# Performance work log

Hardware: AMD Instinct MI355X
Metric: run time of the kernel (lower is better)

Reference implementation:

```python
import jax, jax.numpy as jnp
import numpy as np

EPS = 1e-6
PC_MIN = jnp.array([-50.0, -50.0, -4.0], jnp.float32)
PC_MAX = jnp.array([50.0, 50.0, 4.0], jnp.float32)
IMG_H, IMG_W = 256, 704
G, P, L, D = 1, 8, 4, 128


def _conv3x3(x, w, b):
    y = jax.lax.conv_general_dilated(x, w, (1, 1), ((1, 1), (1, 1)),
                                     dimension_numbers=('NCHW', 'OIHW', 'NCHW'))
    return y + b[None, :, None, None]


def _inorm(x):
    # InstanceNorm2d(affine=False), eps=1e-5, per-sample per-channel over (H,W)
    m = jnp.mean(x, axis=(2, 3), keepdims=True)
    v = jnp.var(x, axis=(2, 3), keepdims=True)
    return (x - m) * jax.lax.rsqrt(v + 1e-5)


def _bilinear(img, xy):
    # img: [H, W, C]; xy: [M, 2] in [0,1] (align_corners=False, zero padding)
    H, W, _ = img.shape
    px = xy[:, 0] * W - 0.5
    py = xy[:, 1] * H - 0.5
    x0 = jnp.floor(px)
    y0 = jnp.floor(py)
    wx = px - x0
    wy = py - y0
    x0 = x0.astype(jnp.int32)
    y0 = y0.astype(jnp.int32)

    def tap(xi, yi, w):
        ok = (xi >= 0) & (xi < W) & (yi >= 0) & (yi < H)
        v = img[jnp.clip(yi, 0, H - 1), jnp.clip(xi, 0, W - 1)]
        return v * (w * ok)[:, None]

    return (tap(x0, y0, (1 - wx) * (1 - wy)) + tap(x0 + 1, y0, wx * (1 - wy)) +
            tap(x0, y0 + 1, (1 - wx) * wy) + tap(x0 + 1, y0 + 1, wx * wy))


def _sampling_4d(pts, feats, scale_w, l2i):
    # pts: [B,Q,G,P,3]; feats: list of [B*G,N,Hl,Wl,C]; scale_w: [B,Q,G,1,P,L]; l2i: [B,N,4,4]
    B, Q, g, p, _ = pts.shape
    N = l2i.shape[1]
    hom = jnp.concatenate([pts, jnp.ones(pts.shape[:-1] + (1,), pts.dtype)], -1)
    cam = jnp.einsum('bnij,bqgpj->bqngpi', l2i, hom)  # project to each camera
    z = cam[..., 2:3]
    xy = cam[..., :2] / jnp.maximum(z, 1e-5)
    xy = xy / jnp.array([IMG_W, IMG_H], xy.dtype)
    xy = jnp.where(z > 1e-5, xy, -1e4)  # behind camera -> samples zero
    xy = jnp.transpose(xy, (0, 3, 2, 1, 4, 5)).reshape(B * g * N, Q * p, 2)
    out = 0.0
    for l, f in enumerate(feats):
        C = f.shape[-1]
        fi = f.reshape(B * g * N, f.shape[2], f.shape[3], C)
        s = jax.vmap(_bilinear)(fi, xy).reshape(B, g, N, Q, p, C).sum(2)  # sum over cameras
        w = jnp.transpose(scale_w[:, :, :, 0, :, l], (0, 2, 1, 3))  # [B,G,Q,P]
        out = out + s * w[..., None]
    return jnp.transpose(out, (0, 2, 1, 3, 4))  # [B,Q,G,P,C]


def _forward(feat0, feat1, feat2, feat3, lidar2img, bev_query, bev_pos,
             in_w, in_b, off_w, off_b, sw_w, sw_b,
             pe_w1, pe_b1, pe_w2, pe_b2,
             mid_w1, mid_b1, mid_w2, mid_b2, mid_w3, mid_b3,
             out_w, out_b):
    B, _, h, w = bev_query.shape
    # decoder prologue: b n (g c) H W -> (b g) n H W c  (G=1)
    feats = [jnp.transpose(f, (0, 1, 3, 4, 2)) for f in (feat0, feat1, feat2, feat3)]
    q = _inorm(bev_query + _conv3x3(bev_query, in_w, in_b))
    qf = jnp.transpose(q, (0, 2, 3, 1)).reshape(B, h * w, D)
    # sampling offsets (1x1 conv as matmul), mode='grid', scale=1.0
    off = jax.nn.sigmoid(qf @ off_w.T + off_b).reshape(B, h * w, G, P, 3)
    lim_xy = 0.25 * 1.0 + EPS
    lim_z = 4.0 + EPS
    off = jnp.concatenate([off[..., :2] * 2 * lim_xy - lim_xy,
                           off[..., 2:3] * 2 * lim_z - lim_z], -1)
    ref = bev_pos.reshape(B, h * w, 1, 1, 3) * (PC_MAX - PC_MIN) + PC_MIN
    pts = ref + off  # [B,Q,G,P,3] in world coords
    sw = (qf @ sw_w.T + sw_b).reshape(B, h * w, G, P, L)[:, :, :, None]  # b q g 1 p l
    sw = jax.nn.softmax(sw, axis=-1)
    sampled = _sampling_4d(pts, feats, sw, lidar2img)  # [B,Q,G,P,128]
    ref_n = (pts - PC_MIN) / (PC_MAX - PC_MIN)
    pe = jax.nn.relu(ref_n @ pe_w1 + pe_b1) @ pe_w2 + pe_b2  # PositionalEncodingMap MLP
    sampled = sampled + pe
    # b (h w) g p c -> b (p g c) h w
    sf = jnp.transpose(sampled, (0, 3, 2, 4, 1)).reshape(B, P * G * 128, h, w)
    m = jax.nn.gelu(jnp.einsum('oi,bihw->bohw', mid_w1, sf) + mid_b1[None, :, None, None], approximate=False)
    m = jax.nn.gelu(jnp.einsum('oi,bihw->bohw', mid_w2, m) + mid_b2[None, :, None, None], approximate=False)
    m = jnp.einsum('oi,bihw->bohw', mid_w3, m) + mid_b3[None, :, None, None]
    q = _inorm(q + m)
    q = _inorm(q + _conv3x3(q, out_w, out_b))
    height = jnp.transpose(off[..., 2], (0, 2, 3, 1)).reshape(B, G, P, h, w)
    return q, height


def _lidar2img_np():
    mats = []
    K = np.array([[500., 0., IMG_W / 2, 0.],
                  [0., 500., IMG_H / 2, 0.],
                  [0., 0., 1., 0.],
                  [0., 0., 0., 1.]])
    for n in range(6):
        th = 2 * np.pi * n / 6
        fwd = np.array([np.cos(th), np.sin(th), 0.])
        right = np.array([-np.sin(th), np.cos(th), 0.])
        down = np.array([0., 0., -1.])
        R = np.stack([right, down, fwd])
        c = fwd * 0.5 + np.array([0., 0., 1.5])
        T = np.eye(4)
        T[:3, :3] = R
        T[:3, 3] = -R @ c
        mats.append(K @ T)
    return np.stack(mats)[None].astype(np.float32)


def setup_inputs():
    key = jax.random.key(0)
    ks = jax.random.split(key, 16)

    def rn(k, shape, s=0.02):
        return jax.random.normal(k, shape, jnp.float32) * s

    B, N, h, w = 1, 6, 128, 128
    return dict(
        feat0=jax.random.normal(ks[0], (B, N, 128, 32, 88), jnp.float32),
        feat1=jax.random.normal(ks[1], (B, N, 128, 16, 44), jnp.float32),
        feat2=jax.random.normal(ks[2], (B, N, 128, 8, 22), jnp.float32),
        feat3=jax.random.normal(ks[3], (B, N, 128, 4, 11), jnp.float32),
        lidar2img=jnp.asarray(_lidar2img_np()),
        bev_query=jax.random.normal(ks[4], (B, 128, h, w), jnp.float32),
        bev_pos=jax.random.uniform(ks[5], (B, h, w, 3), jnp.float32),
        in_w=rn(ks[6], (128, 128, 3, 3)), in_b=jnp.zeros(128, jnp.float32),
        off_w=rn(ks[7], (G * P * 3, 128)),
        off_b=jax.random.uniform(ks[8], (G * P * 3,), jnp.float32, -4.0, 4.0),
        sw_w=rn(ks[9], (G * P * L, 128)), sw_b=jnp.zeros(G * P * L, jnp.float32),
        pe_w1=rn(ks[10], (3, 256), 0.5), pe_b1=jnp.zeros(256, jnp.float32),
        pe_w2=rn(ks[11], (256, 128), 0.1), pe_b2=jnp.zeros(128, jnp.float32),
        mid_w1=rn(ks[12], (512, P * 128)), mid_b1=jnp.zeros(512, jnp.float32),
        mid_w2=rn(ks[13], (512, 512)), mid_b2=jnp.zeros(512, jnp.float32),
        mid_w3=rn(ks[14], (128, 512)), mid_b3=jnp.zeros(128, jnp.float32),
        out_w=rn(ks[15], (128, 128, 3, 3)), out_b=jnp.zeros(128, jnp.float32),
    )


def reference(feat0, feat1, feat2, feat3, lidar2img, bev_query, bev_pos,
              in_w, in_b, off_w, off_b, sw_w, sw_b,
              pe_w1, pe_b1, pe_w2, pe_b2,
              mid_w1, mid_b1, mid_w2, mid_b2, mid_w3, mid_b3,
              out_w, out_b):
    return _forward(feat0, feat1, feat2, feat3, lidar2img, bev_query, bev_pos,
                    in_w, in_b, off_w, off_b, sw_w, sw_b,
                    pe_w1, pe_b1, pe_w2, pe_b2,
                    mid_w1, mid_b1, mid_w2, mid_b2, mid_w3, mid_b3,
                    out_w, out_b)
```

## Files before the change

### kernel.cpp

```cpp
#include <hip/hip_runtime.h>
#include <hip/hip_bf16.h>
#include <math.h>

#define HW 16384

typedef __attribute__((ext_vector_type(8))) short short8;
typedef __attribute__((ext_vector_type(4))) float floatx4;
typedef __attribute__((ext_vector_type(2))) float floatx2;

__device__ __forceinline__ float gelu_exact(float x){
    return 0.5f * x * (1.0f + erff(x * 0.7071067811865475f));
}

__device__ __forceinline__ floatx2 bf2x(unsigned int u){
    floatx2 r;
    r.x = __uint_as_float(u << 16);
    r.y = __uint_as_float(u & 0xffff0000u);
    return r;
}

__global__ __launch_bounds__(256) void feat_transpose_all_k(
    const float* __restrict__ f0, const float* __restrict__ f1,
    const float* __restrict__ f2, const float* __restrict__ f3,
    __hip_bfloat16* __restrict__ out)
{
    int idx = blockIdx.x * 256 + threadIdx.x;
    const float* in; int Hl, Wl, base;
    if (idx < 2162688)      { in = f0; Hl = 32; Wl = 88; base = 0; }
    else if (idx < 2703360) { in = f1; Hl = 16; Wl = 44; base = 2162688; }
    else if (idx < 2838528) { in = f2; Hl = 8;  Wl = 22; base = 2703360; }
    else                    { in = f3; Hl = 4;  Wl = 11; base = 2838528; }
    int r   = idx - base;
    int c   = r & 127;
    int pix = r >> 7;
    int x   = pix % Wl;
    int tt  = pix / Wl;
    int y   = tt % Hl;
    int n   = tt / Hl;
    out[idx] = __float2bfloat16(in[((n * 128 + c) * Hl + y) * Wl + x]);
}

__global__ __launch_bounds__(256) void prep_k(
    const float* __restrict__ mid_w1, const float* __restrict__ mid_w2,
    const float* __restrict__ mid_w3, const float* __restrict__ pe_w2,
    const float* __restrict__ off_w,  const float* __restrict__ off_b,
    const float* __restrict__ sw_w,   const float* __restrict__ sw_b,
    const float* __restrict__ in_w,   const float* __restrict__ out_w,
    __hip_bfloat16* __restrict__ Wb1, __hip_bfloat16* __restrict__ Wb2,
    __hip_bfloat16* __restrict__ Wb3, __hip_bfloat16* __restrict__ Wpe,
    __hip_bfloat16* __restrict__ Wof, float* __restrict__ Bof,
    __hip_bfloat16* __restrict__ Wcv1, __hip_bfloat16* __restrict__ Wcv2)
{
    int b = blockIdx.x, t = threadIdx.x;
    if (b < 2048) {
        int i = b * 256 + t; Wb1[i] = __float2bfloat16(mid_w1[i]);
    } else if (b < 3072) {
        int i = (b - 2048) * 256 + t; Wb2[i] = __float2bfloat16(mid_w2[i]);
    } else if (b < 3328) {
        int i = (b - 3072) * 256 + t; Wb3[i] = __float2bfloat16(mid_w3[i]);
    } else if (b < 3456) {
        int n = b - 3328; Wpe[n * 256 + t] = __float2bfloat16(pe_w2[t * 128 + n]);
    } else if (b < 3584) {
        int n = b - 3456;
        if (t < 128) {
            float w = 0.f;
            if (n < 24)      w = off_w[n * 128 + t];
            else if (n < 56) w = sw_w[(n - 24) * 128 + t];
            Wof[n * 128 + t] = __float2bfloat16(w);
            if (t == 0) Bof[n] = (n < 24) ? off_b[n] : ((n < 56) ? sw_b[n - 24] : 0.f);
        }
    } else if (b < 3712) {
        int o = b - 3584;
        for (int idx = t; idx < 1152; idx += 256) {
            int s = idx >> 7, i = idx & 127;
            Wcv1[o * 1152 + idx] = __float2bfloat16(in_w[(o * 128 + i) * 9 + s]);
        }
    } else {
        int o = b - 3712;
        for (int idx = t; idx < 1152; idx += 256) {
            int s = idx >> 7, i = idx & 127;
            Wcv2[o * 1152 + idx] = __float2bfloat16(out_w[(o * 128 + i) * 9 + s]);
        }
    }
}

__global__ __launch_bounds__(256) void chw2hwc_pad_k(
    const float* __restrict__ q, const float* __restrict__ stats,
    __hip_bfloat16* __restrict__ out)
{
    __shared__ float tile[128][65];
    __shared__ float sm[128], sr[128];
    int t = threadIdx.x;
    if (t < 128) {
        if (stats) {
            float s = stats[2 * t], s2 = stats[2 * t + 1];
            float mean = s * (1.0f / HW);
            sm[t] = mean;
            sr[t] = rsqrtf(s2 * (1.0f / HW) - mean * mean + 1e-5f);
        } else {
            sm[t] = 0.f; sr[t] = 1.f;
        }
    }
    int b = blockIdx.x;
    int y = b >> 1, x0 = (b & 1) * 64;
    int xi = t & 63, c0 = t >> 6;
    for (int c = c0; c < 128; c += 4)
        tile[c][xi] = q[c * HW + y * 128 + x0 + xi];
    __syncthreads();
    int xp = t >> 2, cg = (t & 3) * 32;
    __hip_bfloat16* dst = out + ((size_t)(y + 1) * 130 + (x0 + 1 + xp)) * 128;
    #pragma unroll
    for (int g = 0; g < 4; g++) {
        int c = cg + g * 8;
        union { __hip_bfloat16 h[8]; uint4 u; } pk;
        #pragma unroll
        for (int j = 0; j < 8; j++)
            pk.h[j] = __float2bfloat16((tile[c + j][xp] - sm[c + j]) * sr[c + j]);
        *(uint4*)&dst[c] = pk.u;
    }
}

template<int BM, int BN, int ACT, int OUTT, int CONV>
__global__ __launch_bounds__(256) void bgemm_k(
    const __hip_bfloat16* __restrict__ X, const __hip_bfloat16* __restrict__ W,
    const float* __restrict__ bias, void* __restrict__ outp,
    const float* __restrict__ res,
    const float* __restrict__ rstats, float* __restrict__ ostats,
    int M, int K, int N)
{
    constexpr int ROWS = BM + BN;
    constexpr int ITERS = (ROWS * 4) / 256;
    constexpr int BUFE  = ROWS * 32;
    constexpr int NBUF  = (ITERS == 2) ? 4 : 3;
    __shared__ __align__(16) __hip_bfloat16 SH[NBUF * BUFE];
    int t = threadIdx.x;
    int w = t >> 6, lane = t & 63;
    int mb = blockIdx.y * BM, nb = blockIdx.x * BN;
    int cy = mb >> 7, cx = mb & 127;
    constexpr int WM = BM / 2;
    constexpr int MI = WM / 16;
    constexpr int NJ = BN / 32;
    int wm = (w & 1) * WM, wn = (w >> 1) * (BN / 2);
    int lm = lane & 15, lq = lane >> 4;
    int sl = (lq ^ ((lm >> 1) & 3)) * 8;
    floatx4 zero = {0.f, 0.f, 0.f, 0.f};
    floatx4 acc[MI][NJ];
    #pragma unroll
    for (int i = 0; i < MI; i++)
        #pragma unroll
        for (int j = 0; j < NJ; j++) acc[i][j] = zero;

    const int nsteps = K >> 5;

    auto STAGE = [&](int bufi, int tk2) {
        int kb_ = tk2 * 32;
        int s_ = kb_ >> 7;
        int dyi_ = s_ / 3, dxi_ = s_ - dyi_ * 3;
        #pragma unroll
        for (int it = 0; it < ITERS; it++) {
            int chunk = it * 256 + t;
            int row = chunk >> 2;
            int ko = ((chunk & 3) ^ ((row >> 1) & 3)) * 8;
            const __hip_bfloat16* src;
            if (row < BM) {
                if (CONV)
                    src = X + (((size_t)(cy + dyi_) * 130) + (cx + dxi_ + row)) * 128 + (kb_ & 127) + ko;
                else
                    src = X + (size_t)(mb + row) * K + kb_ + ko;
            } else {
                src = W + (size_t)(nb + row - BM) * K + kb_ + ko;
            }
            __builtin_amdgcn_global_load_lds(
                (const __attribute__((address_space(1))) void*)src,
                (__attribute__((address_space(3))) void*)&SH[bufi * BUFE + (it * 256 + (t & ~63)) * 8],
                16, 0, 0);
        }
    };

    #pragma unroll
    for (int pi = 0; pi < NBUF - 1; pi++)
        if (pi < nsteps) STAGE(pi, pi);

    for (int tk = 0; tk < nsteps; ++tk) {
        int rem = nsteps - 1 - tk;
        if constexpr (ITERS == 2) {
            if (rem >= 2)      asm volatile("s_waitcnt vmcnt(4)" ::: "memory");
            else if (rem == 1) asm volatile("s_waitcnt vmcnt(2)" ::: "memory");
            else               asm volatile("s_waitcnt vmcnt(0)" ::: "memory");
        } else {
            if (rem >= 1)      asm volatile("s_waitcnt vmcnt(4)" ::: "memory");
            else               asm volatile("s_waitcnt vmcnt(0)" ::: "memory");
        }
        __builtin_amdgcn_s_barrier();
        int tkn = tk + NBUF - 1;
        if (tkn < nsteps) STAGE(tkn % NBUF, tkn);

        const __hip_bfloat16* As = SH + (tk % NBUF) * BUFE;
        const __hip_bfloat16* Bs = As + BM * 32;
        short8 af[MI], bf[NJ];
        #pragma unroll
        for (int i = 0; i < MI; i++)
            af[i] = *(const short8*)&As[(wm + i * 16 + lm) * 32 + sl];
        #pragma unroll
        for (int j = 0; j < NJ; j++)
            bf[j] = *(const short8*)&Bs[(wn + j * 16 + lm) * 32 + sl];
        #pragma unroll
        for (int i = 0; i < MI; i++)
            #pragma unroll
            for (int j = 0; j < NJ; j++)
                acc[i][j] = __builtin_amdgcn_mfma_f32_16x16x32_bf16(af[i], bf[j], acc[i][j], 0, 0, 0);
    }

    float invM = 1.0f / (float)M;
    #pragma unroll
    for (int j = 0; j < NJ; j++) {
        int n = nb + wn + j * 16 + lm;
        float bv = bias[n];
        float rmean = 0.f, rrstd = 0.f;
        if (OUTT == 1 && res && rstats) {
            float s = rstats[2 * n], s2 = rstats[2 * n + 1];
            rmean = s * invM;
            rrstd = rsqrtf(s2 * invM - rmean * rmean + 1e-5f);
        }
        float ss = 0.f, ss2 = 0.f;
        #pragma unroll
        for (int i = 0; i < MI; i++) {
            #pragma unroll
            for (int r = 0; r < 4; r++) {
                int m = mb + wm + i * 16 + lq * 4 + r;
                float v = acc[i][j][r] + bv;
                if (ACT) v = gelu_exact(v);
                if (OUTT == 0) {
                    ((__hip_bfloat16*)outp)[(size_t)m * N + n] = __float2bfloat16(v);
                } else {
                    if (res) {
                        float rv = res[(size_t)n * M + m];
                        v += rstats ? (rv - rmean) * rrstd : rv;
                    }
                    ((float*)outp)[(size_t)n * M + m] = v;
                    ss += v; ss2 += v * v;
                }
            }
        }
        if (OUTT == 1 && ostats) {
            ss  += __shfl_xor(ss, 16);  ss  += __shfl_xor(ss, 32);
            ss2 += __shfl_xor(ss2, 16); ss2 += __shfl_xor(ss2, 32);
            if (lq == 0) {
                atomicAdd(&ostats[2 * n], ss);
                atomicAdd(&ostats[2 * n + 1], ss2);
            }
        }
    }
}

__global__ __launch_bounds__(256) void pe_bgemm_k(
    const float* __restrict__ pts, const float* __restrict__ pe_w1,
    const float* __restrict__ pe_b1, const __hip_bfloat16* __restrict__ W,
    const float* __restrict__ bias, __hip_bfloat16* __restrict__ out)
{
    __shared__ __align__(16) __hip_bfloat16 As[128 * 32];
    __shared__ __align__(16) __hip_bfloat16 Bs[128 * 32];
    __shared__ __align__(16) float wps[4][256];
    int t = threadIdx.x;
    int w = t >> 6, lane = t & 63;
    int mb = blockIdx.x * 128;
    {
        int d = t >> 6, c = (t & 63) * 4;
        float4 v;
        if (d == 0) v = *(const float4*)&pe_b1[c];
        else        v = *(const float4*)&pe_w1[(d - 1) * 256 + c];
        *(float4*)&wps[d][c] = v;
    }
    int cg = t & 3;
    int r0 = t >> 2;
    float rn[2][3];
    #pragma unroll
    for (int h = 0; h < 2; h++) {
        int r = mb + r0 + h * 64;
        rn[h][0] = (pts[(size_t)r * 3 + 0] + 50.f) * 0.01f;
        rn[h][1] = (pts[(size_t)r * 3 + 1] + 50.f) * 0.01f;
        rn[h][2] = (pts[(size_t)r * 3 + 2] + 4.f) * 0.125f;
    }
    int wm = (w & 1) * 64, wn = (w >> 1) * 64;
    int lm = lane & 15, lq = lane >> 4;
    floatx4 zero = {0.f, 0.f, 0.f, 0.f};
    floatx4 acc[4][4];
    #pragma unroll
    for (int i = 0; i < 4; i++)
        #pragma unroll
        for (int j = 0; j < 4; j++) acc[i][j] = zero;
    for (int kb = 0; kb < 256; kb += 32) {
        __syncthreads();
        #pragma unroll
        for (int it = 0; it < 2; it++) {
            int chunk = it * 256 + t;
            int brow = chunk >> 2, ko = (chunk & 3) * 8;
            const __hip_bfloat16* src = W + (size_t)brow * 256 + kb + ko;
            __builtin_amdgcn_global_load_lds(
                (const __attribute__((address_space(1))) void*)src,
                (__attribute__((address_space(3))) void*)&Bs[(size_t)(it * 256 + (t & ~63)) * 8],
                16, 0, 0);
        }
        int c0 = kb + cg * 8;
        float4 bva = *(const float4*)&wps[0][c0], bvb = *(const float4*)&wps[0][c0 + 4];
        float4 wxa = *(const float4*)&wps[1][c0], wxb = *(const float4*)&wps[1][c0 + 4];
        float4 wya = *(const float4*)&wps[2][c0], wyb = *(const float4*)&wps[2][c0 + 4];
        float4 wza = *(const float4*)&wps[3][c0], wzb = *(const float4*)&wps[3][c0 + 4];
        #pragma unroll
        for (int h = 0; h < 2; h++) {
            const float* bv = (const float*)&bva;
            const float* wx = (const float*)&wxa;
            const float* wy = (const float*)&wya;
            const float* wz = (const float*)&wza;
            union { __hip_bfloat16 hh[8]; uint4 u; } pk;
            #pragma unroll
            for (int j = 0; j < 4; j++) {
                float v = bv[j] + rn[h][0] * wx[j] + rn[h][1] * wy[j] + rn[h][2] * wz[j];
                pk.hh[j] = __float2bfloat16(fmaxf(v, 0.f));
            }
            bv = (const float*)&bvb; wx = (const float*)&wxb;
            wy = (const float*)&wyb; wz = (const float*)&wzb;
            #pragma unroll
            for (int j = 0; j < 4; j++) {
                float v = bv[j] + rn[h][0] * wx[j] + rn[h][1] * wy[j] + rn[h][2] * wz[j];
                pk.hh[4 + j] = __float2bfloat16(fmaxf(v, 0.f));
            }
            *(uint4*)&As[(r0 + h * 64) * 32 + cg * 8] = pk.u;
        }
        __syncthreads();
        short8 af[4], bf[4];
        #pragma unroll
        for (int i = 0; i < 4; i++)
            af[i] = *(const short8*)&As[(wm + i * 16 + lm) * 32 + lq * 8];
        #pragma unroll
        for (int j = 0; j < 4; j++)
            bf[j] = *(const short8*)&Bs[(wn + j * 16 + lm) * 32 + lq * 8];
        #pragma unroll
        for (int i = 0; i < 4; i++)
            #pragma unroll
            for (int j = 0; j < 4; j++)
                acc[i][j] = __builtin_amdgcn_mfma_f32_16x16x32_bf16(af[i], bf[j], acc[i][j], 0, 0, 0);
    }
    #pragma unroll
    for (int i = 0; i < 4; i++) {
        #pragma unroll
        for (int j = 0; j < 4; j++) {
            int n = wn + j * 16 + lm;
            float bv = bias[n];
            #pragma unroll
            for (int r = 0; r < 4; r++) {
                int m = mb + wm + i * 16 + lq * 4 + r;
                out[(size_t)m * 128 + n] = __float2bfloat16(acc[i][j][r] + bv);
            }
        }
    }
}

__global__ __launch_bounds__(256) void inorm_apply_k(
    const float* __restrict__ in, const float* __restrict__ stats, float* __restrict__ out)
{
    int b = blockIdx.x;
    int c = b >> 3, seg = b & 7;
    float s = stats[2 * c], s2 = stats[2 * c + 1];
    float mean = s * (1.0f / HW);
    float rstd = rsqrtf(s2 * (1.0f / HW) - mean * mean + 1e-5f);
    const float4* pi = (const float4*)(in + (size_t)c * HW + seg * 2048);
    float4*       po = (float4*)(out + (size_t)c * HW + seg * 2048);
    int t = threadIdx.x;
    #pragma unroll
    for (int k = 0; k < 2; k++) {
        float4 v = pi[t + k * 256];
        v.x = (v.x - mean) * rstd; v.y = (v.y - mean) * rstd;
        v.z = (v.z - mean) * rstd; v.w = (v.w - mean) * rstd;
        po[t + k * 256] = v;
    }
}

__global__ __launch_bounds__(256) void offpost_k(
    const float* __restrict__ raw, const float* __restrict__ bev_pos,
    float* __restrict__ pts, float* __restrict__ swn, float* __restrict__ height_out)
{
    int pix = blockIdx.x * 256 + threadIdx.x;
    const float pcmin[3] = {-50.f, -50.f, -4.f};
    const float rng[3]   = {100.f, 100.f, 8.f};
    float bp[3];
    #pragma unroll
    for (int d = 0; d < 3; d++) bp[d] = bev_pos[pix * 3 + d];
    #pragma unroll
    for (int p = 0; p < 8; p++) {
        #pragma unroll
        for (int d = 0; d < 3; d++) {
            float acc = raw[(p * 3 + d) * HW + pix];
            float sv = 1.f / (1.f + expf(-acc));
            float lim = (d == 2) ? (4.0f + 1e-6f) : (0.25f + 1e-6f);
            float offv = sv * 2.f * lim - lim;
            float refv = bp[d] * rng[d] + pcmin[d];
            pts[pix * 24 + p * 3 + d] = refv + offv;
            if (d == 2) height_out[p * HW + pix] = offv;
        }
        float r[4], m = -1e30f;
        #pragma unroll
        for (int l = 0; l < 4; l++) {
            r[l] = raw[(24 + p * 4 + l) * HW + pix];
            m = fmaxf(m, r[l]);
        }
        float sum = 0.f;
        #pragma unroll
        for (int l = 0; l < 4; l++) { r[l] = expf(r[l] - m); sum += r[l]; }
        float inv = 1.f / sum;
        #pragma unroll
        for (int l = 0; l < 4; l++) swn[pix * 32 + p * 4 + l] = r[l] * inv;
    }
}

__global__ __launch_bounds__(256) void sample_k(
    const __hip_bfloat16* __restrict__ featT, const float* __restrict__ pts,
    const float* __restrict__ swn,   const float* __restrict__ l2i,
    __hip_bfloat16* __restrict__ sf)
{
    int pix = blockIdx.x;
    int t = threadIdx.x;
    int lane = t & 63, wv = t >> 6;
    __shared__ float pts_s[24];
    __shared__ float swl_s[32];
    __shared__ float M[96];
    __shared__ __align__(16) int   offs[8][24][4];
    __shared__ __align__(16) float wts[8][24][4];
    __shared__ int cnt[8];
    if (t < 96) M[t] = l2i[t];
    if (t < 24) pts_s[t] = pts[pix * 24 + t];
    if (t < 32) swl_s[t] = swn[pix * 32 + t];
    if (t < 8)  cnt[t] = 0;
    __syncthreads();

    floatx2 acc[2];
    #pragma unroll
    for (int i = 0; i < 2; i++) {
        unsigned int u = *(const unsigned int*)&sf[(size_t)pix * 1024 + (wv * 2 + i) * 128 + 2 * lane];
        acc[i] = bf2x(u);
    }

    const int lHt[4] = {32, 16, 8, 4}, lWt[4] = {88, 44, 22, 11};
    const int loff[4] = {0, 2162688, 2703360, 2838528};
    if (t < 192) {
        int p = t / 24;
        int rr = t - p * 24;
        int n = rr >> 2, l = rr & 3;
        float X = pts_s[p * 3], Y = pts_s[p * 3 + 1], Z = pts_s[p * 3 + 2];
        const float* Mn = &M[n * 16];
        float zc = Mn[8] * X + Mn[9] * Y + Mn[10] * Z + Mn[11];
        if (zc > 1e-5f) {
            float inv = 1.f / zc;
            float xn = (Mn[0] * X + Mn[1] * Y + Mn[2] * Z + Mn[3]) * inv * (1.f / 704.f);
            float yn = (Mn[4] * X + Mn[5] * Y + Mn[6] * Z + Mn[7]) * inv * (1.f / 256.f);
            int Wl = lWt[l], Hl = lHt[l];
            float px = xn * Wl - 0.5f, py = yn * Hl - 0.5f;
            px = fminf(fmaxf(px, -2.f), (float)(Wl + 1));
            py = fminf(fmaxf(py, -2.f), (float)(Hl + 1));
            float x0f = floorf(px), y0f = floorf(py);
            float wx = px - x0f, wy = py - y0f;
            int x0 = (int)x0f, y0 = (int)y0f;
            bool xi0 = (unsigned)x0 < (unsigned)Wl, xi1 = (unsigned)(x0 + 1) < (unsigned)Wl;
            bool yi0 = (unsigned)y0 < (unsigned)Hl, yi1 = (unsigned)(y0 + 1) < (unsigned)Hl;
            if ((xi0 || xi1) && (yi0 || yi1)) {
                float wl = swl_s[p * 4 + l];
                float w00 = wl * (1.f - wx) * (1.f - wy) * (float)(xi0 && yi0);
                float w10 = wl * wx * (1.f - wy)         * (float)(xi1 && yi0);
                float w01 = wl * (1.f - wx) * wy         * (float)(xi0 && yi1);
                float w11 = wl * wx * wy                 * (float)(xi1 && yi1);
                int x0c = min(max(x0, 0), Wl - 1), x1c = min(max(x0 + 1, 0), Wl - 1);
                int y0c = min(max(y0, 0), Hl - 1), y1c = min(max(y0 + 1, 0), Hl - 1);
                int base = loff[l] + n * Hl * Wl * 128;
                int idx = atomicAdd(&cnt[p], 1);
                offs[p][idx][0] = (base + (y0c * Wl + x0c) * 128) * 2;
                offs[p][idx][1] = (base + (y0c * Wl + x1c) * 128) * 2;
                offs[p][idx][2] = (base + (y1c * Wl + x0c) * 128) * 2;
                offs[p][idx][3] = (base + (y1c * Wl + x1c) * 128) * 2;
                wts[p][idx][0] = w00; wts[p][idx][1] = w10;
                wts[p][idx][2] = w01; wts[p][idx][3] = w11;
            }
        }
    }
    __syncthreads();

    const char* fbase = (const char*)featT;
    int lane4 = lane * 4;
    #pragma unroll
    for (int i = 0; i < 2; i++) {
        int p = wv * 2 + i;
        int np = cnt[p];
        floatx2 a0 = acc[i];
        floatx2 a1 = {0.f, 0.f};
        int j = 0;
        #pragma unroll 1
        for (; j + 2 <= np; j += 2) {
            int4   oA = *(const int4*)&offs[p][j][0];
            float4 wA = *(const float4*)&wts[p][j][0];
            int4   oB = *(const int4*)&offs[p][j + 1][0];
            float4 wB = *(const float4*)&wts[p][j + 1][0];
            unsigned int v0 = *(const unsigned int*)(fbase + (unsigned)(oA.x + lane4));
            unsigned int v1 = *(const unsigned int*)(fbase + (unsigned)(oA.y + lane4));
            unsigned int v2 = *(const unsigned int*)(fbase + (unsigned)(oA.z + lane4));
            unsigned int v3 = *(const unsigned int*)(fbase + (unsigned)(oA.w + lane4));
            unsigned int v4 = *(const unsigned int*)(fbase + (unsigned)(oB.x + lane4));
            unsigned int v5 = *(const unsigned int*)(fbase + (unsigned)(oB.y + lane4));
            unsigned int v6 = *(const unsigned int*)(fbase + (unsigned)(oB.z + lane4));
            unsigned int v7 = *(const unsigned int*)(fbase + (unsigned)(oB.w + lane4));
            a0 += bf2x(v0) * wA.x;
            a0 += bf2x(v1) * wA.y;
            a0 += bf2x(v2) * wA.z;
            a0 += bf2x(v3) * wA.w;
            a1 += bf2x(v4) * wB.x;
            a1 += bf2x(v5) * wB.y;
            a1 += bf2x(v6) * wB.z;
            a1 += bf2x(v7) * wB.w;
        }
        if (j < np) {
            int4   o = *(const int4*)&offs[p][j][0];
            float4 w = *(const float4*)&wts[p][j][0];
            unsigned int v0 = *(const unsigned int*)(fbase + (unsigned)(o.x + lane4));
            unsigned int v1 = *(const unsigned int*)(fbase + (unsigned)(o.y + lane4));
            unsigned int v2 = *(const unsigned int*)(fbase + (unsigned)(o.z + lane4));
            unsigned int v3 = *(const unsigned int*)(fbase + (unsigned)(o.w + lane4));
            a0 += bf2x(v0) * w.x;
            a0 += bf2x(v1) * w.y;
            a0 += bf2x(v2) * w.z;
            a0 += bf2x(v3) * w.w;
        }
        acc[i] = a0 + a1;
    }
    #pragma unroll
    for (int i = 0; i < 2; i++) {
        union { __hip_bfloat16 h[2]; unsigned int u; } pk;
        pk.h[0] = __float2bfloat16(acc[i].x);
        pk.h[1] = __float2bfloat16(acc[i].y);
        *(unsigned int*)&sf[(size_t)pix * 1024 + (wv * 2 + i) * 128 + 2 * lane] = pk.u;
    }
}

extern "C" void kernel_launch(void* const* d_in, const int* in_sizes, int n_in,
                              void* d_out, int out_size, void* d_ws, size_t ws_size,
                              hipStream_t stream)
{
    const float* feat[4] = {(const float*)d_in[0], (const float*)d_in[1],
                            (const float*)d_in[2], (const float*)d_in[3]};
    const float* l2i       = (const float*)d_in[4];
    const float* bev_query = (const float*)d_in[5];
    const float* bev_pos   = (const float*)d_in[6];
    const float* in_w  = (const float*)d_in[7];  const float* in_b  = (const float*)d_in[8];
    const float* off_w = (const float*)d_in[9];  const float* off_b = (const float*)d_in[10];
    const float* sw_w  = (const float*)d_in[11]; const float* sw_b  = (const float*)d_in[12];
    const float* pe_w1 = (const float*)d_in[13]; const float* pe_b1 = (const float*)d_in[14];
    const float* pe_w2 = (const float*)d_in[15]; const float* pe_b2 = (const float*)d_in[16];
    const float* mid_w1 = (const float*)d_in[17]; const float* mid_b1 = (const float*)d_in[18];
    const float* mid_w2 = (const float*)d_in[19]; const float* mid_b2 = (const float*)d_in[20];
    const float* mid_w3 = (const float*)d_in[21]; const float* mid_b3 = (const float*)d_in[22];
    const float* out_w  = (const float*)d_in[23]; const float* out_b  = (const float*)d_in[24];

    float* ws = (float*)d_ws;
    float* fTf = ws;
    __hip_bfloat16* fT = (__hip_bfloat16*)fTf;
    float* Bb  = fTf + 1436160;
    float* Cb  = Bb + 2097152;
    float* Gb  = Cb + 2097152;
    float* Dp  = Gb + 2097152;
    float* Eb  = Dp + 393216;
    float* QTf = Eb + 524288;
    __hip_bfloat16* qT = (__hip_bfloat16*)QTf;
    float* SFf = QTf + 1081600;
    __hip_bfloat16* sfb = (__hip_bfloat16*)SFf;
    float* M1f = SFf + 8388608;
    __hip_bfloat16* m1b = (__hip_bfloat16*)M1f;
    float* M2f = M1f + 4194304;
    __hip_bfloat16* m2b = (__hip_bfloat16*)M2f;
    float* WC1 = M2f + 4194304;
    __hip_bfloat16* Wcv1 = (__hip_bfloat16*)WC1;
    float* WC2 = WC1 + 73728;
    __hip_bfloat16* Wcv2 = (__hip_bfloat16*)WC2;
    float* W1f = WC2 + 73728;
    __hip_bfloat16* Wb1 = (__hip_bfloat16*)W1f;
    float* W2f = W1f + 262144;
    __hip_bfloat16* Wb2 = (__hip_bfloat16*)W2f;
    float* W3f = W2f + 131072;
    __hip_bfloat16* Wb3 = (__hip_bfloat16*)W3f;
    float* WPf = W3f + 32768;
    __hip_bfloat16* Wpe = (__hip_bfloat16*)WPf;
    float* WOf = WPf + 16384;
    __hip_bfloat16* Wof = (__hip_bfloat16*)WOf;
    float* Bof = WOf + 8192;
    float* Stats = Bof + 128;
    float* stats1 = Stats;
    float* stats2 = Stats + 256;
    float* stats3 = Stats + 512;

    float* q_out = (float*)d_out;
    float* h_out = q_out + 2097152;

    hipMemsetAsync(qT, 0, (size_t)130 * 130 * 128 * sizeof(__hip_bfloat16), stream);
    hipMemsetAsync(Stats, 0, 768 * sizeof(float), stream);

    feat_transpose_all_k<<<11220, 256, 0, stream>>>(feat[0], feat[1], feat[2], feat[3], fT);
    prep_k<<<3840, 256, 0, stream>>>(mid_w1, mid_w2, mid_w3, pe_w2, off_w, off_b, sw_w, sw_b,
                                     in_w, out_w, Wb1, Wb2, Wb3, Wpe, Wof, Bof, Wcv1, Wcv2);

    chw2hwc_pad_k<<<256, 256, 0, stream>>>(bev_query, nullptr, qT);
    bgemm_k<64, 64, 0, 1, 1><<<dim3(2, 256), 256, 0, stream>>>(
        qT, Wcv1, in_b, Cb, bev_query, nullptr, stats1, HW, 1152, 128);

    chw2hwc_pad_k<<<256, 256, 0, stream>>>(Cb, stats1, qT);
    bgemm_k<64, 64, 0, 1, 1><<<dim3(2, 256), 256, 0, stream>>>(
        qT + 131 * 128, Wof, Bof, Bb, nullptr, nullptr, nullptr, HW, 128, 128);
    offpost_k<<<64, 256, 0, stream>>>(Bb, bev_pos, Dp, Eb, h_out);

    pe_bgemm_k<<<1024, 256, 0, stream>>>(Dp, pe_w1, pe_b1, Wpe, pe_b2, sfb);

    sample_k<<<HW, 256, 0, stream>>>(fT, Dp, Eb, l2i, sfb);

    bgemm_k<128, 128, 1, 0, 0><<<dim3(4, 128), 256, 0, stream>>>(
        sfb, Wb1, mid_b1, m1b, nullptr, nullptr, nullptr, HW, 1024, 512);
    bgemm_k<128, 128, 1, 0, 0><<<dim3(4, 128), 256, 0, stream>>>(
        m1b, Wb2, mid_b2, m2b, nullptr, nullptr, nullptr, HW, 512, 512);
    bgemm_k<64, 64, 0, 1, 0><<<dim3(2, 256), 256, 0, stream>>>(
        m2b, Wb3, mid_b3, Bb, Cb, stats1, stats2, HW, 512, 128);

    chw2hwc_pad_k<<<256, 256, 0, stream>>>(Bb, stats2, qT);
    bgemm_k<64, 64, 0, 1, 1><<<dim3(2, 256), 256, 0, stream>>>(
        qT, Wcv2, out_b, Gb, Bb, stats2, stats3, HW, 1152, 128);
    inorm_apply_k<<<1024, 256, 0, stream>>>(Gb, stats3, q_out);
}
```

Measured before the change: 395.4 us.

## Tile feature transpose through LDS and widen bilinear gathers to 16-byte loads

The feature NCHW-to-NHWC bf16 conversion now stages a row of 128 channels in shared memory, so global reads are coalesced and each thread writes 16-byte packed outputs. It replaces the per-element strided gather with 552 blocks. The sampling kernel splits each wavefront into four 16-lane quarters, one per bilinear tap, with each lane loading 8 bf16 channels via uint4. The quarters are then combined with cross-lane shuffles, cutting the number of gather instructions at the cost of shuffle reductions and lower lane utilisation on the final store.

```diff
diff --git a/kernel.cpp b/kernel.cpp
--- a/kernel.cpp
+++ b/kernel.cpp
@@ -19,25 +19,56 @@
     return r;
 }
 
+__device__ __forceinline__ float foldq(float v){
+    v += __shfl_xor(v, 16);
+    v += __shfl_xor(v, 32);
+    return v;
+}
+
+template<int CW, int HL, int WL>
+__device__ __forceinline__ void ft_tile(
+    float* tile, const float* __restrict__ in, __hip_bfloat16* __restrict__ out,
+    int n, int y, int x0, int base, int t)
+{
+    const float* src = in + ((size_t)n * 128 * HL + y) * WL + x0;
+    constexpr int NE = 128 * CW;
+    for (int idx = t; idx < NE; idx += 256) {
+        int c = idx / CW, x = idx - c * CW;
+        tile[c * 45 + x] = src[(size_t)c * (HL * WL) + x];
+    }
+    __syncthreads();
+    __hip_bfloat16* dst = out + base + ((size_t)(n * HL + y) * WL + x0) * 128;
+    constexpr int NO = CW * 16;
+    for (int idx = t; idx < NO; idx += 256) {
+        int x = idx >> 4, g = idx & 15;
+        union { __hip_bfloat16 h[8]; uint4 u; } pk;
+        #pragma unroll
+        for (int jj = 0; jj < 8; jj++)
+            pk.h[jj] = __float2bfloat16(tile[(g * 8 + jj) * 45 + x]);
+        *(uint4*)&dst[(size_t)x * 128 + g * 8] = pk.u;
+    }
+}
+
 __global__ __launch_bounds__(256) void feat_transpose_all_k(
     const float* __restrict__ f0, const float* __restrict__ f1,
     const float* __restrict__ f2, const float* __restrict__ f3,
     __hip_bfloat16* __restrict__ out)
 {
-    int idx = blockIdx.x * 256 + threadIdx.x;
-    const float* in; int Hl, Wl, base;
-    if (idx < 2162688)      { in = f0; Hl = 32; Wl = 88; base = 0; }
-    else if (idx < 2703360) { in = f1; Hl = 16; Wl = 44; base = 2162688; }
-    else if (idx < 2838528) { in = f2; Hl = 8;  Wl = 22; base = 2703360; }
-    else                    { in = f3; Hl = 4;  Wl = 11; base = 2838528; }
-    int r   = idx - base;
-    int c   = r & 127;
-    int pix = r >> 7;
-    int x   = pix % Wl;
-    int tt  = pix / Wl;
-    int y   = tt % Hl;
-    int n   = tt / Hl;
-    out[idx] = __float2bfloat16(in[((n * 128 + c) * Hl + y) * Wl + x]);
+    __shared__ float tile[128 * 45];
+    int b = blockIdx.x, t = threadIdx.x;
+    if (b < 384) {
+        int n = b >> 6, q = b & 63, y = q >> 1, x0 = (q & 1) * 44;
+        ft_tile<44, 32, 88>(tile, f0, out, n, y, x0, 0, t);
+    } else if (b < 480) {
+        int r = b - 384, n = r >> 4, y = r & 15;
+        ft_tile<44, 16, 44>(tile, f1, out, n, y, 0, 2162688, t);
+    } else if (b < 528) {
+        int r = b - 480, n = r >> 3, y = r & 7;
+        ft_tile<22, 8, 22>(tile, f2, out, n, y, 0, 2703360, t);
+    } else {
+        int r = b - 528, n = r >> 2, y = r & 3;
+        ft_tile<11, 4, 11>(tile, f3, out, n, y, 0, 2838528, t);
+    }
 }
 
 __global__ __launch_bounds__(256) void prep_k(
@@ -421,6 +452,7 @@
     int pix = blockIdx.x;
     int t = threadIdx.x;
     int lane = t & 63, wv = t >> 6;
+    int qq = lane >> 4, lq = lane & 15;
     __shared__ float pts_s[24];
     __shared__ float swl_s[32];
     __shared__ float M[96];
@@ -433,11 +465,17 @@
     if (t < 8)  cnt[t] = 0;
     __syncthreads();
 
-    floatx2 acc[2];
+    floatx2 ac[2][4];
     #pragma unroll
     for (int i = 0; i < 2; i++) {
-        unsigned int u = *(const unsigned int*)&sf[(size_t)pix * 1024 + (wv * 2 + i) * 128 + 2 * lane];
-        acc[i] = bf2x(u);
+        if (qq == 0) {
+            uint4 u = *(const uint4*)&sf[(size_t)pix * 1024 + (wv * 2 + i) * 128 + 8 * lq];
+            ac[i][0] = bf2x(u.x); ac[i][1] = bf2x(u.y);
+            ac[i][2] = bf2x(u.z); ac[i][3] = bf2x(u.w);
+        } else {
+            floatx2 z = {0.f, 0.f};
+            ac[i][0] = z; ac[i][1] = z; ac[i][2] = z; ac[i][3] = z;
+        }
     }
 
     const int lHt[4] = {32, 16, 8, 4}, lWt[4] = {88, 44, 22, 11};
@@ -484,57 +522,52 @@
     __syncthreads();
 
     const char* fbase = (const char*)featT;
-    int lane4 = lane * 4;
+    int lq16 = lq * 16;
     #pragma unroll
     for (int i = 0; i < 2; i++) {
         int p = wv * 2 + i;
         int np = cnt[p];
-        floatx2 a0 = acc[i];
-        floatx2 a1 = {0.f, 0.f};
+        floatx2 b0 = ac[i][0], b1 = ac[i][1], b2 = ac[i][2], b3 = ac[i][3];
+        floatx2 c0 = {0.f,0.f}, c1 = {0.f,0.f}, c2 = {0.f,0.f}, c3 = {0.f,0.f};
         int j = 0;
         #pragma unroll 1
         for (; j + 2 <= np; j += 2) {
-            int4   oA = *(const int4*)&offs[p][j][0];
-            float4 wA = *(const float4*)&wts[p][j][0];
-            int4   oB = *(const int4*)&offs[p][j + 1][0];
-            float4 wB = *(const float4*)&wts[p][j + 1][0];
-            unsigned int v0 = *(const unsigned int*)(fbase + (unsigned)(oA.x + lane4));
-            unsigned int v1 = *(const unsigned int*)(fbase + (unsigned)(oA.y + lane4));
-            unsigned int v2 = *(const unsigned int*)(fbase + (unsigned)(oA.z + lane4));
-            unsigned int v3 = *(const unsigned int*)(fbase + (unsigned)(oA.w + lane4));
-            unsigned int v4 = *(const unsigned int*)(fbase + (unsigned)(oB.x + lane4));
-            unsigned int v5 = *(const unsigned int*)(fbase + (unsigned)(oB.y + lane4));
-            unsigned int v6 = *(const unsigned int*)(fbase + (unsigned)(oB.z + lane4));
-            unsigned int v7 = *(const unsigned int*)(fbase + (unsigned)(oB.w + lane4));
-            a0 += bf2x(v0) * wA.x;
-            a0 += bf2x(v1) * wA.y;
-            a0 += bf2x(v2) * wA.z;
-            a0 += bf2x(v3) * wA.w;
-            a1 += bf2x(v4) * wB.x;
-            a1 += bf2x(v5) * wB.y;
-            a1 += bf2x(v6) * wB.z;
-            a1 += bf2x(v7) * wB.w;
+            int   oA = offs[p][j][qq];
+            float wA = wts[p][j][qq];
+            int   oB = offs[p][j + 1][qq];
+            float wB = wts[p][j + 1][qq];
+            uint4 vA = *(const uint4*)(fbase + (unsigned)(oA + lq16));
+            uint4 vB = *(const uint4*)(fbase + (unsigned)(oB + lq16));
+            b0 += bf2x(vA.x) * wA; b1 += bf2x(vA.y) * wA;
+            b2 += bf2x(vA.z) * wA; b3 += bf2x(vA.w) * wA;
+            c0 += bf2x(vB.x) * wB; c1 += bf2x(vB.y) * wB;
+            c2 += bf2x(vB.z) * wB; c3 += bf2x(vB.w) * wB;
         }
         if (j < np) {
-            int4   o = *(const int4*)&offs[p][j][0];
-            float4 w = *(const float4*)&wts[p][j][0];
-            unsigned int v0 = *(const unsigned int*)(fbase + (unsigned)(o.x + lane4));
-            unsigned int v1 = *(const unsigned int*)(fbase + (unsigned)(o.y + lane4));
-            unsigned int v2 = *(const unsigned int*)(fbase + (unsigned)(o.z + lane4));
-            unsigned int v3 = *(const unsigned int*)(fbase + (unsigned)(o.w + lane4));
-            a0 += bf2x(v0) * w.x;
-            a0 += bf2x(v1) * w.y;
-            a0 += bf2x(v2) * w.z;
-            a0 += bf2x(v3) * w.w;
-        }
-        acc[i] = a0 + a1;
-    }
-    #pragma unroll
-    for (int i = 0; i < 2; i++) {
-        union { __hip_bfloat16 h[2]; unsigned int u; } pk;
-        pk.h[0] = __float2bfloat16(acc[i].x);
-        pk.h[1] = __float2bfloat16(acc[i].y);
-        *(unsigned int*)&sf[(size_t)pix * 1024 + (wv * 2 + i) * 128 + 2 * lane] = pk.u;
+            int   o = offs[p][j][qq];
+            float w0 = wts[p][j][qq];
+            uint4 v = *(const uint4*)(fbase + (unsigned)(o + lq16));
+            b0 += bf2x(v.x) * w0; b1 += bf2x(v.y) * w0;
+            b2 += bf2x(v.z) * w0; b3 += bf2x(v.w) * w0;
+        }
+        b0 += c0; b1 += c1; b2 += c2; b3 += c3;
+        b0.x = foldq(b0.x); b0.y = foldq(b0.y);
+        b1.x = foldq(b1.x); b1.y = foldq(b1.y);
+        b2.x = foldq(b2.x); b2.y = foldq(b2.y);
+        b3.x = foldq(b3.x); b3.y = foldq(b3.y);
+        ac[i][0] = b0; ac[i][1] = b1; ac[i][2] = b2; ac[i][3] = b3;
+    }
+    if (qq < 2) {
+        floatx2 s0 = qq ? ac[1][0] : ac[0][0];
+        floatx2 s1 = qq ? ac[1][1] : ac[0][1];
+        floatx2 s2 = qq ? ac[1][2] : ac[0][2];
+        floatx2 s3 = qq ? ac[1][3] : ac[0][3];
+        union { __hip_bfloat16 h[8]; uint4 u; } pk;
+        pk.h[0] = __float2bfloat16(s0.x); pk.h[1] = __float2bfloat16(s0.y);
+        pk.h[2] = __float2bfloat16(s1.x); pk.h[3] = __float2bfloat16(s1.y);
+        pk.h[4] = __float2bfloat16(s2.x); pk.h[5] = __float2bfloat16(s2.y);
+        pk.h[6] = __float2bfloat16(s3.x); pk.h[7] = __float2bfloat16(s3.y);
+        *(uint4*)&sf[(size_t)pix * 1024 + (wv * 2 + qq) * 128 + 8 * lq] = pk.u;
     }
 }
 
@@ -599,7 +632,7 @@
     hipMemsetAsync(qT, 0, (size_t)130 * 130 * 128 * sizeof(__hip_bfloat16), stream);
     hipMemsetAsync(Stats, 0, 768 * sizeof(float), stream);
 
-    feat_transpose_all_k<<<11220, 256, 0, stream>>>(feat[0], feat[1], feat[2], feat[3], fT);
+    feat_transpose_all_k<<<552, 256, 0, stream>>>(feat[0], feat[1], feat[2], feat[3], fT);
     prep_k<<<3840, 256, 0, stream>>>(mid_w1, mid_w2, mid_w3, pe_w2, off_w, off_b, sw_w, sw_b,
                                      in_w, out_w, Wb1, Wb2, Wb3, Wpe, Wof, Bof, Wcv1, Wcv2);
 
```

New measurement: 401.5 us. About the same (+1.6%).

## Tile feature transpose through shared memory and widen sampling blocks to one wave per point

Applied to the files above, without the earlier changes.

The feature NCHW-to-NHWC bf16 transpose now stages one image row of 128 channels in shared memory. It then writes 16-byte packed bf16 vectors, replacing a per-element kernel that did strided scalar reads. The sampling kernel moves to 512 threads so each of the 8 wavefronts handles one sampling point instead of two, which doubles in-flight gathers per block. It also remaps block index to pixel so neighbouring blocks land on different parts of the BEV grid. Larger blocks may reduce occupancy, and the pixel remap changes cache locality for the feature gathers.

```diff
diff --git a/kernel.cpp b/kernel.cpp
--- a/kernel.cpp
+++ b/kernel.cpp
@@ -19,25 +19,50 @@
     return r;
 }
 
+template<int CW, int HL, int WL>
+__device__ __forceinline__ void ft_tile(
+    float* tile, const float* __restrict__ in, __hip_bfloat16* __restrict__ out,
+    int n, int y, int x0, int base, int t)
+{
+    const float* src = in + ((size_t)n * 128 * HL + y) * WL + x0;
+    constexpr int NE = 128 * CW;
+    for (int idx = t; idx < NE; idx += 256) {
+        int c = idx / CW, x = idx - c * CW;
+        tile[c * 45 + x] = src[(size_t)c * (HL * WL) + x];
+    }
+    __syncthreads();
+    __hip_bfloat16* dst = out + base + ((size_t)(n * HL + y) * WL + x0) * 128;
+    constexpr int NO = CW * 16;
+    for (int idx = t; idx < NO; idx += 256) {
+        int x = idx >> 4, g = idx & 15;
+        union { __hip_bfloat16 h[8]; uint4 u; } pk;
+        #pragma unroll
+        for (int jj = 0; jj < 8; jj++)
+            pk.h[jj] = __float2bfloat16(tile[(g * 8 + jj) * 45 + x]);
+        *(uint4*)&dst[(size_t)x * 128 + g * 8] = pk.u;
+    }
+}
+
 __global__ __launch_bounds__(256) void feat_transpose_all_k(
     const float* __restrict__ f0, const float* __restrict__ f1,
     const float* __restrict__ f2, const float* __restrict__ f3,
     __hip_bfloat16* __restrict__ out)
 {
-    int idx = blockIdx.x * 256 + threadIdx.x;
-    const float* in; int Hl, Wl, base;
-    if (idx < 2162688)      { in = f0; Hl = 32; Wl = 88; base = 0; }
-    else if (idx < 2703360) { in = f1; Hl = 16; Wl = 44; base = 2162688; }
-    else if (idx < 2838528) { in = f2; Hl = 8;  Wl = 22; base = 2703360; }
-    else                    { in = f3; Hl = 4;  Wl = 11; base = 2838528; }
-    int r   = idx - base;
-    int c   = r & 127;
-    int pix = r >> 7;
-    int x   = pix % Wl;
-    int tt  = pix / Wl;
-    int y   = tt % Hl;
-    int n   = tt / Hl;
-    out[idx] = __float2bfloat16(in[((n * 128 + c) * Hl + y) * Wl + x]);
+    __shared__ float tile[128 * 45];
+    int b = blockIdx.x, t = threadIdx.x;
+    if (b < 384) {
+        int n = b >> 6, q = b & 63, y = q >> 1, x0 = (q & 1) * 44;
+        ft_tile<44, 32, 88>(tile, f0, out, n, y, x0, 0, t);
+    } else if (b < 480) {
+        int r = b - 384, n = r >> 4, y = r & 15;
+        ft_tile<44, 16, 44>(tile, f1, out, n, y, 0, 2162688, t);
+    } else if (b < 528) {
+        int r = b - 480, n = r >> 3, y = r & 7;
+        ft_tile<22, 8, 22>(tile, f2, out, n, y, 0, 2703360, t);
+    } else {
+        int r = b - 528, n = r >> 2, y = r & 3;
+        ft_tile<11, 4, 11>(tile, f3, out, n, y, 0, 2838528, t);
+    }
 }
 
 __global__ __launch_bounds__(256) void prep_k(
@@ -413,12 +438,13 @@
     }
 }
 
-__global__ __launch_bounds__(256) void sample_k(
+__global__ __launch_bounds__(512) void sample_k(
     const __hip_bfloat16* __restrict__ featT, const float* __restrict__ pts,
     const float* __restrict__ swn,   const float* __restrict__ l2i,
     __hip_bfloat16* __restrict__ sf)
 {
-    int pix = blockIdx.x;
+    int bid = blockIdx.x;
+    int pix = (bid & 7) * 2048 + (bid >> 3);
     int t = threadIdx.x;
     int lane = t & 63, wv = t >> 6;
     __shared__ float pts_s[24];
@@ -433,11 +459,10 @@
     if (t < 8)  cnt[t] = 0;
     __syncthreads();
 
-    floatx2 acc[2];
-    #pragma unroll
-    for (int i = 0; i < 2; i++) {
-        unsigned int u = *(const unsigned int*)&sf[(size_t)pix * 1024 + (wv * 2 + i) * 128 + 2 * lane];
-        acc[i] = bf2x(u);
+    floatx2 acc;
+    {
+        unsigned int u = *(const unsigned int*)&sf[(size_t)pix * 1024 + wv * 128 + 2 * lane];
+        acc = bf2x(u);
     }
 
     const int lHt[4] = {32, 16, 8, 4}, lWt[4] = {88, 44, 22, 11};
@@ -485,11 +510,10 @@
 
     const char* fbase = (const char*)featT;
     int lane4 = lane * 4;
-    #pragma unroll
-    for (int i = 0; i < 2; i++) {
-        int p = wv * 2 + i;
+    {
+        int p = wv;
         int np = cnt[p];
-        floatx2 a0 = acc[i];
+        floatx2 a0 = acc;
         floatx2 a1 = {0.f, 0.f};
         int j = 0;
         #pragma unroll 1
@@ -527,14 +551,13 @@
             a0 += bf2x(v2) * w.z;
             a0 += bf2x(v3) * w.w;
         }
-        acc[i] = a0 + a1;
-    }
-    #pragma unroll
-    for (int i = 0; i < 2; i++) {
+        acc = a0 + a1;
+    }
+    {
         union { __hip_bfloat16 h[2]; unsigned int u; } pk;
-        pk.h[0] = __float2bfloat16(acc[i].x);
-        pk.h[1] = __float2bfloat16(acc[i].y);
-        *(unsigned int*)&sf[(size_t)pix * 1024 + (wv * 2 + i) * 128 + 2 * lane] = pk.u;
+        pk.h[0] = __float2bfloat16(acc.x);
+        pk.h[1] = __float2bfloat16(acc.y);
+        *(unsigned int*)&sf[(size_t)pix * 1024 + wv * 128 + 2 * lane] = pk.u;
     }
 }
 
@@ -599,7 +622,7 @@
     hipMemsetAsync(qT, 0, (size_t)130 * 130 * 128 * sizeof(__hip_bfloat16), stream);
     hipMemsetAsync(Stats, 0, 768 * sizeof(float), stream);
 
-    feat_transpose_all_k<<<11220, 256, 0, stream>>>(feat[0], feat[1], feat[2], feat[3], fT);
+    feat_transpose_all_k<<<552, 256, 0, stream>>>(feat[0], feat[1], feat[2], feat[3], fT);
     prep_k<<<3840, 256, 0, stream>>>(mid_w1, mid_w2, mid_w3, pe_w2, off_w, off_b, sw_w, sw_b,
                                      in_w, out_w, Wb1, Wb2, Wb3, Wpe, Wof, Bof, Wcv1, Wcv2);
 
@@ -614,7 +637,7 @@
 
     pe_bgemm_k<<<1024, 256, 0, stream>>>(Dp, pe_w1, pe_b1, Wpe, pe_b2, sfb);
 
-    sample_k<<<HW, 256, 0, stream>>>(fT, Dp, Eb, l2i, sfb);
+    sample_k<<<HW, 512, 0, stream>>>(fT, Dp, Eb, l2i, sfb);
 
     bgemm_k<128, 128, 1, 0, 0><<<dim3(4, 128), 256, 0, stream>>>(
         sfb, Wb1, mid_b1, m1b, nullptr, nullptr, nullptr, HW, 1024, 512);
```

Result: slower. 404.0 us (+2.2%).
